# Optimization experiments

Measured on AMD Instinct MI355X. Metric: run time of the kernel, lower is better.

## Reference

```python
import jax, jax.numpy as jnp
import numpy as np

B, LQ, LK = 4, 4096, 4096
D = 1024          # num_heads * key_dim = 16 * 64
Q_DIM = 1024      # query_dim
K_DIM = 1024      # note: linear_k input dim; here inputs carry d_model features
V_DIM = 1024      # value_dim


def setup_inputs() -> dict:
    key = jax.random.key(0)
    ks = jax.random.split(key, 12)
    s_in = 1.0 / np.sqrt(Q_DIM)
    s_d = 1.0 / np.sqrt(D)
    return {
        "q": jax.random.normal(ks[0], (B, LQ, Q_DIM), jnp.float32),
        "k": jax.random.normal(ks[1], (B, LK, K_DIM), jnp.float32),
        "v": jax.random.normal(ks[2], (B, LK, V_DIM), jnp.float32),
        # Linear weights stored [in, out] so projection is x @ W + b
        "Wq": jax.random.normal(ks[3], (Q_DIM, D), jnp.float32) * s_in,
        "bq": jax.random.normal(ks[4], (D,), jnp.float32) * s_in,
        "Wk": jax.random.normal(ks[5], (K_DIM, D), jnp.float32) * s_in,
        "bk": jax.random.normal(ks[6], (D,), jnp.float32) * s_in,
        "Wv": jax.random.normal(ks[7], (V_DIM, D), jnp.float32) * s_in,
        "bv": jax.random.normal(ks[8], (D,), jnp.float32) * s_in,
        "Wo": jax.random.normal(ks[9], (D, V_DIM), jnp.float32) * s_d,
        "bo": jax.random.normal(ks[10], (V_DIM,), jnp.float32) * s_d,
    }


def reference(q, k, v, Wq, bq, Wk, bk, Wv, bv, Wo, bo):
    # Projections: [B, L, D]
    qp = jax.nn.softmax(q @ Wq + bq, axis=-1)   # softmax over feature dim
    kp = jax.nn.softmax(k @ Wk + bk, axis=-2)   # softmax over sequence dim
    vp = jax.nn.softmax(v @ Wv + bv, axis=-2)   # softmax over sequence dim
    # Dropout is identity in eval mode (module uses dropout_p at train only).
    scores = jnp.einsum("bqd,bkd->bqk", qp, kp)  # [B, LQ, LK]
    ctx = jnp.einsum("bqk,bkd->bqd", scores, vp)  # [B, LQ, D]
    return ctx @ Wo + bo                          # [B, LQ, V_DIM]
```

## Files before the change

kernel.cpp:

```cpp
#include <hip/hip_runtime.h>

typedef _Float16 f16x8 __attribute__((ext_vector_type(8)));
typedef float f32x4 __attribute__((ext_vector_type(4)));
typedef long lx2 __attribute__((ext_vector_type(2)));

__device__ __forceinline__ float h2f(unsigned short h) {
  return (float)__builtin_bit_cast(_Float16, h);
}
__device__ __forceinline__ unsigned short f2h(float f) {
  return __builtin_bit_cast(unsigned short, (_Float16)f);
}
__device__ __forceinline__ unsigned char f2e4(float f) {
  unsigned short h = __builtin_bit_cast(unsigned short, (_Float16)f);
  unsigned s = (h >> 8) & 0x80u;
  unsigned ae = h & 0x7FFFu;
  if (ae >= 0x5F00u) return (unsigned char)(s | 0x7Eu);
  if (ae >= 0x2400u) {
    unsigned t = ae - 0x2000u;
    t = (t + 0x3Fu + ((t >> 7) & 1u)) >> 7;
    return (unsigned char)(s | t);
  }
  float v = (float)__builtin_bit_cast(_Float16, (unsigned short)ae) * 512.0f;
  int n = (int)rintf(v);
  return (unsigned char)(s | (unsigned)n);
}
__device__ __forceinline__ unsigned pk4e4(float a, float b, float c, float d) {
  return (unsigned)f2e4(a) | ((unsigned)f2e4(b) << 8) |
         ((unsigned)f2e4(c) << 16) | ((unsigned)f2e4(d) << 24);
}

__device__ __forceinline__ void gload_lds16(const void* g, void* l) {
  __builtin_amdgcn_global_load_lds(
      (const __attribute__((address_space(1))) void*)g,
      (__attribute__((address_space(3))) void*)l, 16, 0, 0);
}

template <int DT, int ASRC, int OUTMODE>
__global__ __launch_bounds__(512, 4) void gemmt(
    const void* __restrict__ Av, const void* __restrict__ Btv,
    void* __restrict__ Cv, const float* __restrict__ bias,
    float* __restrict__ sums,
    int N, int K, int ldk, int gx, int gy, int nsplit,
    long sA, long sB, long sC)
{
  __shared__ alignas(16) unsigned char smem[49152];
  const int tid  = threadIdx.x;
  const int lane = tid & 63;
  const int wave = tid >> 6;
  const int waveM = wave >> 2;
  const int waveN = wave & 3;
  const int EB = (DT == 1) ? 1 : 2;

  const int nwg = (int)gridDim.x;
  const int cpx = nwg >> 3;
  const int wg  = (int)blockIdx.x;
  const int w   = (wg & 7) * cpx + (wg >> 3);
  const int x   = w % gx;
  const int rem = w / gx;
  const int y   = rem % gy;
  const int zt  = rem / gy;
  const int bz  = zt / nsplit;
  const int sp  = zt % nsplit;

  const int m0 = y * 128, n0 = x * 256;
  const size_t ldkB = (size_t)ldk * EB;
  const size_t ldkB64 = ldkB * 64, ldkB128 = ldkB * 128;

  const int srow = tid >> 3;
  const int scol = ((tid * 16) & 127) ^ ((srow & 7) << 4);
  const char* ApR16 = nullptr;
  const char* ApR32 = nullptr;
  const char* BpR;
  {
    const char* Bb = (const char*)Btv + ((long)bz * sB + (long)sp * K) * EB
                     + (size_t)n0 * ldkB;
    BpR = Bb + (size_t)srow * ldkB + scol;
    if (ASRC == 0) {
      const char* Ab = (const char*)Av + ((long)bz * sA + (long)sp * K) * EB
                       + (size_t)m0 * ldkB;
      ApR16 = Ab + (size_t)srow * ldkB + scol;
    } else {
      const char* Ab = (const char*)Av + ((long)bz * sA + (long)sp * K) * 4
                       + (size_t)m0 * (size_t)ldk * 4;
      ApR32 = Ab + (size_t)srow * (size_t)ldk * 4 + (size_t)scol * 2;
    }
  }
  const unsigned oA0 = (unsigned)tid * 16;
  const size_t ldk32_64 = (size_t)ldk * 4 * 64;

  int offA[4], offB[4];
  {
    const int q16 = (lane >> 4) << 4;
#pragma unroll
    for (int mi = 0; mi < 4; ++mi) {
      const int r = waveM * 64 + mi * 16 + (lane & 15);
      offA[mi] = r * 128 + (q16 ^ ((r & 7) << 4));
    }
#pragma unroll
    for (int ni = 0; ni < 4; ++ni) {
      const int r = waveN * 64 + ni * 16 + (lane & 15);
      offB[ni] = 16384 + r * 128 + (q16 ^ ((r & 7) << 4));
    }
  }

  f32x4 acc[4][4] = {};

  float4 pf0, pf1, pf2, pf3;
  if (ASRC == 1) {
    const char* s0 = ApR32;
    const char* s1 = s0 + ldk32_64;
    pf0 = *(const float4*)s0;  pf1 = *(const float4*)(s0 + 16);
    pf2 = *(const float4*)s1;  pf3 = *(const float4*)(s1 + 16);
  }

  const int nk = (DT == 1) ? (K >> 7) : (K >> 6);
  for (int kt = 0; kt < nk; ++kt) {
    const size_t kb = (size_t)kt * 128;
    if (ASRC == 0) {
      gload_lds16(ApR16 + kb,           smem + oA0);
      gload_lds16(ApR16 + ldkB64 + kb,  smem + oA0 + 8192);
    } else {
      unsigned short h0[8], h1[8];
      const float* fa0 = (const float*)&pf0; const float* fa1 = (const float*)&pf1;
      const float* fb0 = (const float*)&pf2; const float* fb1 = (const float*)&pf3;
#pragma unroll
      for (int e = 0; e < 4; ++e) {
        h0[e] = f2h(fa0[e]); h0[4 + e] = f2h(fa1[e]);
        h1[e] = f2h(fb0[e]); h1[4 + e] = f2h(fb1[e]);
      }
      *(uint4*)&smem[oA0]        = *(const uint4*)h0;
      *(uint4*)&smem[oA0 + 8192] = *(const uint4*)h1;
      if (kt + 1 < nk) {
        const char* s0 = ApR32 + (size_t)(kt + 1) * 256;
        const char* s1 = s0 + ldk32_64;
        pf0 = *(const float4*)s0;  pf1 = *(const float4*)(s0 + 16);
        pf2 = *(const float4*)s1;  pf3 = *(const float4*)(s1 + 16);
      }
    }
    gload_lds16(BpR + kb,                     smem + 16384 + oA0);
    gload_lds16(BpR + ldkB64 + kb,            smem + 16384 + oA0 + 8192);
    gload_lds16(BpR + ldkB128 + kb,           smem + 16384 + oA0 + 16384);
    gload_lds16(BpR + ldkB128 + ldkB64 + kb,  smem + 16384 + oA0 + 24576);
    __syncthreads();
#pragma unroll
    for (int kk = 0; kk < 2; ++kk) {
      const int kx = kk << 6;
      if (DT == 0) {
        f16x8 aF[4], bF[4];
#pragma unroll
        for (int mi = 0; mi < 4; ++mi) aF[mi] = *(const f16x8*)&smem[offA[mi] ^ kx];
#pragma unroll
        for (int ni = 0; ni < 4; ++ni) bF[ni] = *(const f16x8*)&smem[offB[ni] ^ kx];
#pragma unroll
        for (int mi = 0; mi < 4; ++mi)
#pragma unroll
          for (int ni = 0; ni < 4; ++ni)
            acc[mi][ni] = __builtin_amdgcn_mfma_f32_16x16x32_f16(aF[mi], bF[ni], acc[mi][ni], 0, 0, 0);
      } else {
        lx2 aF[4], bF[4];
#pragma unroll
        for (int mi = 0; mi < 4; ++mi) aF[mi] = *(const lx2*)&smem[offA[mi] ^ kx];
#pragma unroll
        for (int ni = 0; ni < 4; ++ni) bF[ni] = *(const lx2*)&smem[offB[ni] ^ kx];
#pragma unroll
        for (int h = 0; h < 2; ++h)
#pragma unroll
          for (int mi = 0; mi < 4; ++mi)
#pragma unroll
            for (int ni = 0; ni < 4; ++ni)
              acc[mi][ni] = __builtin_amdgcn_mfma_f32_16x16x32_fp8_fp8(
                  aF[mi][h], bF[ni][h], acc[mi][ni], 0, 0, 0);
      }
    }
    __syncthreads();
  }

  const int rb = (lane >> 4) * 4;
  const int cb_ = lane & 15;
  const long zout = (OUTMODE == 2) ? (long)zt : (long)bz;

  if (OUTMODE == 3) {
#pragma unroll
    for (int m = 0; m < 4; ++m) {
      const int row0 = m0 + waveM * 64 + m * 16 + rb;
      float rs0 = 0, rs1 = 0, rs2 = 0, rs3 = 0;
#pragma unroll
      for (int n = 0; n < 4; ++n) {
        const int col = n0 + waveN * 64 + n * 16 + cb_;
        const float badd = bias[col];
        const float e0 = __expf(acc[m][n][0] + badd);
        const float e1 = __expf(acc[m][n][1] + badd);
        const float e2 = __expf(acc[m][n][2] + badd);
        const float e3 = __expf(acc[m][n][3] + badd);
        unsigned char* C8 = (unsigned char*)Cv + zout * sC;
        C8[(size_t)(row0 + 0) * N + col] = f2e4(e0 * 0.0625f);
        C8[(size_t)(row0 + 1) * N + col] = f2e4(e1 * 0.0625f);
        C8[(size_t)(row0 + 2) * N + col] = f2e4(e2 * 0.0625f);
        C8[(size_t)(row0 + 3) * N + col] = f2e4(e3 * 0.0625f);
        rs0 += e0; rs1 += e1; rs2 += e2; rs3 += e3;
      }
#pragma unroll
      for (int off = 1; off <= 8; off <<= 1) {
        rs0 += __shfl_xor(rs0, off);
        rs1 += __shfl_xor(rs1, off);
        rs2 += __shfl_xor(rs2, off);
        rs3 += __shfl_xor(rs3, off);
      }
      if ((lane & 15) == 0) {
        float* s = sums + (size_t)zout * 4096 + row0;
        atomicAdd(s + 0, rs0);
        atomicAdd(s + 1, rs1);
        atomicAdd(s + 2, rs2);
        atomicAdd(s + 3, rs3);
      }
    }
  } else if (OUTMODE == 4) {
    float cs[4] = {0.f, 0.f, 0.f, 0.f};
#pragma unroll
    for (int m = 0; m < 4; ++m) {
      const int row0 = m0 + waveM * 64 + m * 16 + rb;
#pragma unroll
      for (int n = 0; n < 4; ++n) {
        const int col = n0 + waveN * 64 + n * 16 + cb_;
        const float badd = bias[col];
        float ev[4];
        float ls = 0.f;
#pragma unroll
        for (int r = 0; r < 4; ++r) {
          ev[r] = __expf(acc[m][n][r] + badd);
          ls += ev[r];
        }
        cs[n] += ls;
        *(unsigned*)((unsigned char*)Cv + zout * sC + ((size_t)col << 12) + row0) =
            pk4e4(ev[0] * 0.0625f, ev[1] * 0.0625f, ev[2] * 0.0625f, ev[3] * 0.0625f);
      }
    }
#pragma unroll
    for (int n = 0; n < 4; ++n) {
      cs[n] += __shfl_xor(cs[n], 16);
      cs[n] += __shfl_xor(cs[n], 32);
    }
    if (lane < 16) {
#pragma unroll
      for (int n = 0; n < 4; ++n) {
        const int col = n0 + waveN * 64 + n * 16 + lane;
        atomicAdd(sums + ((size_t)zout << 10) + col, cs[n]);
      }
    }
  } else {
#pragma unroll
    for (int m = 0; m < 4; ++m) {
      const int row0 = m0 + waveM * 64 + m * 16 + rb;
      float i0 = 0, i1 = 0, i2 = 0, i3 = 0;
      if (OUTMODE == 5) {
        const float4 s4 = *(const float4*)&sums[(size_t)zout * 4096 + row0];
        i0 = 1.0f / (256.0f * s4.x); i1 = 1.0f / (256.0f * s4.y);
        i2 = 1.0f / (256.0f * s4.z); i3 = 1.0f / (256.0f * s4.w);
      }
#pragma unroll
      for (int n = 0; n < 4; ++n) {
        const int col = n0 + waveN * 64 + n * 16 + cb_;
        if (OUTMODE == 2) {
#pragma unroll
          for (int r = 0; r < 4; ++r)
            ((unsigned short*)Cv)[zout * sC + (size_t)(row0 + r) * N + col] = f2h(acc[m][n][r]);
        } else if (OUTMODE == 5) {
          const float badd = bias[col];
          float* C32 = (float*)Cv;
          C32[zout * sC + (size_t)(row0 + 0) * N + col] = acc[m][n][0] * i0 + badd;
          C32[zout * sC + (size_t)(row0 + 1) * N + col] = acc[m][n][1] * i1 + badd;
          C32[zout * sC + (size_t)(row0 + 2) * N + col] = acc[m][n][2] * i2 + badd;
          C32[zout * sC + (size_t)(row0 + 3) * N + col] = acc[m][n][3] * i3 + badd;
        } else {
          const float badd = bias[col];
#pragma unroll
          for (int r = 0; r < 4; ++r)
            ((float*)Cv)[zout * sC + (size_t)(row0 + r) * N + col] = acc[m][n][r] + badd;
        }
      }
    }
  }
}

__global__ __launch_bounds__(256) void w_trh4(
    const float* __restrict__ W0, const float* __restrict__ W1,
    const float* __restrict__ W2, const float* __restrict__ W3,
    unsigned short* __restrict__ WTb)
{
  __shared__ unsigned short tile[64][73];
  const int z = blockIdx.z;
  const float* W = (z == 0) ? W0 : (z == 1) ? W1 : (z == 2) ? W2 : W3;
  unsigned short* WT = WTb + (size_t)z * 1024 * 1024;
  const int c0 = blockIdx.x * 64;
  const int r0 = blockIdx.y * 64;
  const int tid = threadIdx.x;
  const int r = tid >> 2;
  const int cq = (tid & 3) * 16;
#pragma unroll
  for (int i = 0; i < 4; ++i) {
    const int c = cq + i * 4;
    const float4 v = *(const float4*)&W[(size_t)(r0 + r) * 1024 + c0 + c];
    tile[r][c + 0] = f2h(v.x);
    tile[r][c + 1] = f2h(v.y);
    tile[r][c + 2] = f2h(v.z);
    tile[r][c + 3] = f2h(v.w);
  }
  __syncthreads();
  const int c = tid >> 2;
  const int rq = (tid & 3) * 16;
  unsigned short outv[16];
#pragma unroll
  for (int j = 0; j < 16; ++j) outv[j] = tile[rq + j][c];
  unsigned short* Tb = WT + (size_t)(c0 + c) * 1024 + r0 + rq;
  ((uint4*)Tb)[0] = ((const uint4*)outv)[0];
  ((uint4*)Tb)[1] = ((const uint4*)outv)[1];
}

__global__ __launch_bounds__(256) void wo8k(
    const unsigned short* __restrict__ WoT, unsigned char* __restrict__ WoT8)
{
  const int i = blockIdx.x * 256 + threadIdx.x;
  const uint2 u = ((const uint2*)WoT)[i];
  ((unsigned*)WoT8)[i] = pk4e4(h2f(u.x & 0xffff) * 8.f, h2f(u.x >> 16) * 8.f,
                               h2f(u.y & 0xffff) * 8.f, h2f(u.y >> 16) * 8.f);
}

__global__ __launch_bounds__(256) void red4m(
    const unsigned short* __restrict__ P, const float* __restrict__ skr,
    const float* __restrict__ svr, unsigned char* __restrict__ O)
{
  const int i = blockIdx.x * 256 + threadIdx.x;
  const int b = i >> 18;
  const int j = i & 262143;
  const int dk = j >> 8;
  const int dv0 = (j & 255) << 2;
  float s0 = 0, s1 = 0, s2 = 0, s3 = 0;
#pragma unroll
  for (int sl = 0; sl < 4; ++sl) {
    const uint2 u = *(const uint2*)(P + (((long)(b * 4 + sl)) << 20) + ((long)j << 2));
    s0 += h2f(u.x & 0xffff); s1 += h2f(u.x >> 16);
    s2 += h2f(u.y & 0xffff); s3 += h2f(u.y >> 16);
  }
  const float fk = 4194304.0f / skr[(b << 10) + dk];
  const float4 fv = *(const float4*)&svr[(b << 10) + dv0];
  ((unsigned*)O)[i] = pk4e4(s0 * fk / fv.x, s1 * fk / fv.y,
                            s2 * fk / fv.z, s3 * fk / fv.w);
}

__global__ __launch_bounds__(256) void red4g(
    const unsigned short* __restrict__ P, unsigned char* __restrict__ O)
{
  const int i = blockIdx.x * 256 + threadIdx.x;
  const int b = i >> 18;
  const int j = i & 262143;
  float s0 = 0, s1 = 0, s2 = 0, s3 = 0;
#pragma unroll
  for (int sl = 0; sl < 4; ++sl) {
    const uint2 u = *(const uint2*)(P + (((long)(b * 4 + sl)) << 20) + ((long)j << 2));
    s0 += h2f(u.x & 0xffff); s1 += h2f(u.x >> 16);
    s2 += h2f(u.y & 0xffff); s3 += h2f(u.y >> 16);
  }
  ((unsigned*)O)[i] = pk4e4(s0 * 0.03125f, s1 * 0.03125f,
                            s2 * 0.03125f, s3 * 0.03125f);
}

extern "C" void kernel_launch(void* const* d_in, const int* in_sizes, int n_in,
                              void* d_out, int out_size, void* d_ws, size_t ws_size,
                              hipStream_t stream) {
  const float* q  = (const float*)d_in[0];
  const float* k  = (const float*)d_in[1];
  const float* v  = (const float*)d_in[2];
  const float* Wq = (const float*)d_in[3];
  const float* bq = (const float*)d_in[4];
  const float* Wk = (const float*)d_in[5];
  const float* bk = (const float*)d_in[6];
  const float* Wv = (const float*)d_in[7];
  const float* bv = (const float*)d_in[8];
  const float* Wo = (const float*)d_in[9];
  const float* bo = (const float*)d_in[10];
  float* out = (float*)d_out;

  char* p = (char*)d_ws;
  unsigned short* Part = (unsigned short*)p; p += 33554432;
  unsigned short* WTb  = (unsigned short*)p; p += 8388608;
  unsigned short* WqT = WTb;
  unsigned short* WkT = WTb + 1L * 1024 * 1024;
  unsigned short* WvT = WTb + 2L * 1024 * 1024;
  unsigned short* WoT = WTb + 3L * 1024 * 1024;
  unsigned char* WoT8 = (unsigned char*)p;   p += 1048576;
  unsigned char* Eq8  = (unsigned char*)p;   p += 16777216;
  unsigned char* ETk8 = (unsigned char*)p;   p += 16777216;
  unsigned char* ETv8 = (unsigned char*)p;   p += 16777216;
  unsigned char* Mh8  = (unsigned char*)p;   p += 4194304;
  unsigned char* GT8  = (unsigned char*)p;   p += 4194304;
  float* sqraw = (float*)p; p += 16384 * 4;
  float* skraw = (float*)p; p += 4096 * 4;
  float* svraw = (float*)p; p += 4096 * 4;

  const dim3 blk(256);
  const dim3 blk512(512);
  const long S22 = 4096L * 1024;
  const long S20 = 1024L * 1024;

  hipMemsetAsync(sqraw, 0, (16384 + 4096 + 4096) * sizeof(float), stream);

  w_trh4<<<dim3(16, 16, 4), blk, 0, stream>>>(Wq, Wk, Wv, Wo, WTb);
  wo8k<<<1024, blk, 0, stream>>>(WoT, WoT8);

  gemmt<0, 1, 3><<<512, blk512, 0, stream>>>(q, WqT, Eq8, bq, sqraw,
      1024, 1024, 1024, 4, 32, 1, S22, 0, S22);

  gemmt<0, 1, 4><<<512, blk512, 0, stream>>>(k, WkT, ETk8, bk, skraw,
      1024, 1024, 1024, 4, 32, 1, S22, 0, S22);

  gemmt<0, 1, 4><<<512, blk512, 0, stream>>>(v, WvT, ETv8, bv, svraw,
      1024, 1024, 1024, 4, 32, 1, S22, 0, S22);

  gemmt<1, 0, 2><<<512, blk512, 0, stream>>>(ETk8, ETv8, Part, nullptr, nullptr,
      1024, 1024, 4096, 4, 8, 4, S22, S22, S20);
  red4m<<<4096, blk, 0, stream>>>(Part, skraw, svraw, Mh8);

  gemmt<1, 0, 2><<<512, blk512, 0, stream>>>(WoT8, Mh8, Part, nullptr, nullptr,
      1024, 256, 1024, 4, 8, 4, 0, S20, S20);
  red4g<<<4096, blk, 0, stream>>>(Part, GT8);

  gemmt<1, 0, 5><<<512, blk512, 0, stream>>>(Eq8, GT8, out, bo, sqraw,
      1024, 1024, 1024, 4, 32, 1, S22, S20, S22);

  (void)in_sizes; (void)n_in; (void)out_size; (void)ws_size;
}
```

Baseline: 280.9 us.

## Merge three projection GEMMs into one launch, use hardware FP8 conversion

Replaces the three separate Q/K/V projection launches with a single proj3 kernel of 1536 workgroups that selects input, weights, bias and epilogue per workgroup. This removes launch gaps and tail effects between the projections. The software float-to-e4m3 conversion is replaced with the cvt_pk_fp8_f32 builtin when the compiler provides it, and the Wo FP8 conversion is folded into the weight transpose kernel, which removes one launch. Risks are small rounding differences from the hardware conversion (saturation and NaN handling) and some divergence from the per-workgroup pointer selection.

Measured after the change: 263.0 us. 1.07x faster.

```diff
diff --git a/kernel.cpp b/kernel.cpp
--- a/kernel.cpp
+++ b/kernel.cpp
@@ -10,7 +10,14 @@
 __device__ __forceinline__ unsigned short f2h(float f) {
   return __builtin_bit_cast(unsigned short, (_Float16)f);
 }
-__device__ __forceinline__ unsigned char f2e4(float f) {
+
+#if __has_builtin(__builtin_amdgcn_cvt_pk_fp8_f32)
+#define HW_FP8 1
+#else
+#define HW_FP8 0
+#endif
+
+__device__ __forceinline__ unsigned char f2e4_sw(float f) {
   unsigned short h = __builtin_bit_cast(unsigned short, (_Float16)f);
   unsigned s = (h >> 8) & 0x80u;
   unsigned ae = h & 0x7FFFu;
@@ -24,9 +31,22 @@
   int n = (int)rintf(v);
   return (unsigned char)(s | (unsigned)n);
 }
+
+__device__ __forceinline__ unsigned pk2e4(float a, float b) {
+#if HW_FP8
+  return (unsigned)__builtin_amdgcn_cvt_pk_fp8_f32(a, b, 0, false) & 0xFFFFu;
+#else
+  return (unsigned)f2e4_sw(a) | ((unsigned)f2e4_sw(b) << 8);
+#endif
+}
 __device__ __forceinline__ unsigned pk4e4(float a, float b, float c, float d) {
-  return (unsigned)f2e4(a) | ((unsigned)f2e4(b) << 8) |
-         ((unsigned)f2e4(c) << 16) | ((unsigned)f2e4(d) << 24);
+#if HW_FP8
+  int lo = __builtin_amdgcn_cvt_pk_fp8_f32(a, b, 0, false);
+  return (unsigned)__builtin_amdgcn_cvt_pk_fp8_f32(c, d, lo, true);
+#else
+  return (unsigned)f2e4_sw(a) | ((unsigned)f2e4_sw(b) << 8) |
+         ((unsigned)f2e4_sw(c) << 16) | ((unsigned)f2e4_sw(d) << 24);
+#endif
 }
 
 __device__ __forceinline__ void gload_lds16(const void* g, void* l) {
@@ -35,11 +55,194 @@
       (__attribute__((address_space(3))) void*)l, 16, 0, 0);
 }
 
-template <int DT, int ASRC, int OUTMODE>
-__global__ __launch_bounds__(512, 4) void gemmt(
-    const void* __restrict__ Av, const void* __restrict__ Btv,
+__global__ __launch_bounds__(512, 4) void proj3(
+    const float* __restrict__ A0, const float* __restrict__ A1,
+    const float* __restrict__ A2, const unsigned short* __restrict__ WTb,
+    const float* __restrict__ b0, const float* __restrict__ b1,
+    const float* __restrict__ b2, unsigned char* __restrict__ C0,
+    unsigned char* __restrict__ C1, unsigned char* __restrict__ C2,
+    float* __restrict__ s0, float* __restrict__ s1, float* __restrict__ s2)
+{
+  __shared__ alignas(16) unsigned char smem[49152];
+  const int tid  = threadIdx.x;
+  const int lane = tid & 63;
+  const int wave = tid >> 6;
+  const int waveM = wave >> 2;
+  const int waveN = wave & 3;
+
+  const int wg = (int)blockIdx.x;
+  const int w  = (wg & 7) * 192 + (wg >> 3);
+  const int z  = w / 512;
+  const int wl = w - z * 512;
+  const int x  = wl & 3;
+  const int rem = wl >> 2;
+  const int y  = rem & 31;
+  const int bz = rem >> 5;
+
+  const float* Af = (z == 0) ? A0 : (z == 1) ? A1 : A2;
+  const float* bi = (z == 0) ? b0 : (z == 1) ? b1 : b2;
+  unsigned char* Cp = (z == 0) ? C0 : (z == 1) ? C1 : C2;
+  float* sums = (z == 0) ? s0 : (z == 1) ? s1 : s2;
+
+  const int m0 = y * 128, n0 = x * 256;
+
+  const int srow = tid >> 3;
+  const int scol = ((tid * 16) & 127) ^ ((srow & 7) << 4);
+  const char* BpR = (const char*)(WTb + (size_t)z * 1048576)
+                    + (size_t)n0 * 2048 + (size_t)srow * 2048 + scol;
+  const char* ApR32 = (const char*)Af + (size_t)bz * (4096L * 1024 * 4)
+                      + (size_t)m0 * 4096 + (size_t)srow * 4096 + (size_t)scol * 2;
+  const unsigned oA0 = (unsigned)tid * 16;
+
+  int offA[4], offB[4];
+  {
+    const int q16 = (lane >> 4) << 4;
+#pragma unroll
+    for (int mi = 0; mi < 4; ++mi) {
+      const int r = waveM * 64 + mi * 16 + (lane & 15);
+      offA[mi] = r * 128 + (q16 ^ ((r & 7) << 4));
+    }
+#pragma unroll
+    for (int ni = 0; ni < 4; ++ni) {
+      const int r = waveN * 64 + ni * 16 + (lane & 15);
+      offB[ni] = 16384 + r * 128 + (q16 ^ ((r & 7) << 4));
+    }
+  }
+
+  f32x4 acc[4][4] = {};
+
+  float4 pf0, pf1, pf2, pf3;
+  {
+    const char* sa = ApR32;
+    const char* sb = sa + 4096 * 64;
+    pf0 = *(const float4*)sa;  pf1 = *(const float4*)(sa + 16);
+    pf2 = *(const float4*)sb;  pf3 = *(const float4*)(sb + 16);
+  }
+
+  for (int kt = 0; kt < 16; ++kt) {
+    const size_t kb = (size_t)kt * 128;
+    {
+      unsigned short h0[8], h1[8];
+      const float* fa0 = (const float*)&pf0; const float* fa1 = (const float*)&pf1;
+      const float* fb0 = (const float*)&pf2; const float* fb1 = (const float*)&pf3;
+#pragma unroll
+      for (int e = 0; e < 4; ++e) {
+        h0[e] = f2h(fa0[e]); h0[4 + e] = f2h(fa1[e]);
+        h1[e] = f2h(fb0[e]); h1[4 + e] = f2h(fb1[e]);
+      }
+      *(uint4*)&smem[oA0]        = *(const uint4*)h0;
+      *(uint4*)&smem[oA0 + 8192] = *(const uint4*)h1;
+      if (kt + 1 < 16) {
+        const char* sa = ApR32 + (size_t)(kt + 1) * 256;
+        const char* sb = sa + 4096 * 64;
+        pf0 = *(const float4*)sa;  pf1 = *(const float4*)(sa + 16);
+        pf2 = *(const float4*)sb;  pf3 = *(const float4*)(sb + 16);
+      }
+    }
+    gload_lds16(BpR + kb,                      smem + 16384 + oA0);
+    gload_lds16(BpR + 2048 * 64 + kb,          smem + 16384 + oA0 + 8192);
+    gload_lds16(BpR + 2048 * 128 + kb,         smem + 16384 + oA0 + 16384);
+    gload_lds16(BpR + 2048 * 192 + kb,         smem + 16384 + oA0 + 24576);
+    __syncthreads();
+#pragma unroll
+    for (int kk = 0; kk < 2; ++kk) {
+      const int kx = kk << 6;
+      f16x8 aF[4], bF[4];
+#pragma unroll
+      for (int mi = 0; mi < 4; ++mi) aF[mi] = *(const f16x8*)&smem[offA[mi] ^ kx];
+#pragma unroll
+      for (int ni = 0; ni < 4; ++ni) bF[ni] = *(const f16x8*)&smem[offB[ni] ^ kx];
+#pragma unroll
+      for (int mi = 0; mi < 4; ++mi)
+#pragma unroll
+        for (int ni = 0; ni < 4; ++ni)
+          acc[mi][ni] = __builtin_amdgcn_mfma_f32_16x16x32_f16(aF[mi], bF[ni], acc[mi][ni], 0, 0, 0);
+    }
+    __syncthreads();
+  }
+
+  const int rb = (lane >> 4) * 4;
+  const int cb_ = lane & 15;
+  const long sC = 4096L * 1024;
+
+  if (z == 0) {
+#pragma unroll
+    for (int m = 0; m < 4; ++m) {
+      const int row0 = m0 + waveM * 64 + m * 16 + rb;
+      float rs0 = 0, rs1 = 0, rs2 = 0, rs3 = 0;
+#pragma unroll
+      for (int n = 0; n < 4; ++n) {
+        const int col = n0 + waveN * 64 + n * 16 + cb_;
+        const float badd = bi[col];
+        const float e0 = __expf(acc[m][n][0] + badd);
+        const float e1 = __expf(acc[m][n][1] + badd);
+        const float e2 = __expf(acc[m][n][2] + badd);
+        const float e3 = __expf(acc[m][n][3] + badd);
+        const unsigned p01 = pk2e4(e0 * 0.0625f, e1 * 0.0625f);
+        const unsigned p23 = pk2e4(e2 * 0.0625f, e3 * 0.0625f);
+        unsigned char* C8 = Cp + (long)bz * sC;
+        C8[(size_t)(row0 + 0) * 1024 + col] = (unsigned char)(p01 & 0xff);
+        C8[(size_t)(row0 + 1) * 1024 + col] = (unsigned char)((p01 >> 8) & 0xff);
+        C8[(size_t)(row0 + 2) * 1024 + col] = (unsigned char)(p23 & 0xff);
+        C8[(size_t)(row0 + 3) * 1024 + col] = (unsigned char)((p23 >> 8) & 0xff);
+        rs0 += e0; rs1 += e1; rs2 += e2; rs3 += e3;
+      }
+#pragma unroll
+      for (int off = 1; off <= 8; off <<= 1) {
+        rs0 += __shfl_xor(rs0, off);
+        rs1 += __shfl_xor(rs1, off);
+        rs2 += __shfl_xor(rs2, off);
+        rs3 += __shfl_xor(rs3, off);
+      }
+      if ((lane & 15) == 0) {
+        float* s = sums + (size_t)bz * 4096 + row0;
+        atomicAdd(s + 0, rs0);
+        atomicAdd(s + 1, rs1);
+        atomicAdd(s + 2, rs2);
+        atomicAdd(s + 3, rs3);
+      }
+    }
+  } else {
+    float cs[4] = {0.f, 0.f, 0.f, 0.f};
+#pragma unroll
+    for (int m = 0; m < 4; ++m) {
+      const int row0 = m0 + waveM * 64 + m * 16 + rb;
+#pragma unroll
+      for (int n = 0; n < 4; ++n) {
+        const int col = n0 + waveN * 64 + n * 16 + cb_;
+        const float badd = bi[col];
+        float ev[4];
+        float ls = 0.f;
+#pragma unroll
+        for (int r = 0; r < 4; ++r) {
+          ev[r] = __expf(acc[m][n][r] + badd);
+          ls += ev[r];
+        }
+        cs[n] += ls;
+        *(unsigned*)(Cp + (long)bz * sC + ((size_t)col << 12) + row0) =
+            pk4e4(ev[0] * 0.0625f, ev[1] * 0.0625f, ev[2] * 0.0625f, ev[3] * 0.0625f);
+      }
+    }
+#pragma unroll
+    for (int n = 0; n < 4; ++n) {
+      cs[n] += __shfl_xor(cs[n], 16);
+      cs[n] += __shfl_xor(cs[n], 32);
+    }
+    if (lane < 16) {
+#pragma unroll
+      for (int n = 0; n < 4; ++n) {
+        const int col = n0 + waveN * 64 + n * 16 + lane;
+        atomicAdd(sums + ((size_t)bz << 10) + col, cs[n]);
+      }
+    }
+  }
+}
+
+template <int OUTMODE>
+__global__ __launch_bounds__(512, 4) void gemm8(
+    const unsigned char* __restrict__ A, const unsigned char* __restrict__ Bt,
     void* __restrict__ Cv, const float* __restrict__ bias,
-    float* __restrict__ sums,
+    const float* __restrict__ sums,
     int N, int K, int ldk, int gx, int gy, int nsplit,
     long sA, long sB, long sC)
 {
@@ -49,7 +252,6 @@
   const int wave = tid >> 6;
   const int waveM = wave >> 2;
   const int waveN = wave & 3;
-  const int EB = (DT == 1) ? 1 : 2;
 
   const int nwg = (int)gridDim.x;
   const int cpx = nwg >> 3;
@@ -63,30 +265,20 @@
   const int sp  = zt % nsplit;
 
   const int m0 = y * 128, n0 = x * 256;
-  const size_t ldkB = (size_t)ldk * EB;
+  const size_t ldkB = (size_t)ldk;
   const size_t ldkB64 = ldkB * 64, ldkB128 = ldkB * 128;
 
   const int srow = tid >> 3;
   const int scol = ((tid * 16) & 127) ^ ((srow & 7) << 4);
-  const char* ApR16 = nullptr;
-  const char* ApR32 = nullptr;
+  const char* ApR;
   const char* BpR;
   {
-    const char* Bb = (const char*)Btv + ((long)bz * sB + (long)sp * K) * EB
-                     + (size_t)n0 * ldkB;
+    const char* Ab = (const char*)A + (long)bz * sA + (long)sp * K + (size_t)m0 * ldkB;
+    const char* Bb = (const char*)Bt + (long)bz * sB + (long)sp * K + (size_t)n0 * ldkB;
+    ApR = Ab + (size_t)srow * ldkB + scol;
     BpR = Bb + (size_t)srow * ldkB + scol;
-    if (ASRC == 0) {
-      const char* Ab = (const char*)Av + ((long)bz * sA + (long)sp * K) * EB
-                       + (size_t)m0 * ldkB;
-      ApR16 = Ab + (size_t)srow * ldkB + scol;
-    } else {
-      const char* Ab = (const char*)Av + ((long)bz * sA + (long)sp * K) * 4
-                       + (size_t)m0 * (size_t)ldk * 4;
-      ApR32 = Ab + (size_t)srow * (size_t)ldk * 4 + (size_t)scol * 2;
-    }
   }
   const unsigned oA0 = (unsigned)tid * 16;
-  const size_t ldk32_64 = (size_t)ldk * 4 * 64;
 
   int offA[4], offB[4];
   {
@@ -105,38 +297,11 @@
 
   f32x4 acc[4][4] = {};
 
-  float4 pf0, pf1, pf2, pf3;
-  if (ASRC == 1) {
-    const char* s0 = ApR32;
-    const char* s1 = s0 + ldk32_64;
-    pf0 = *(const float4*)s0;  pf1 = *(const float4*)(s0 + 16);
-    pf2 = *(const float4*)s1;  pf3 = *(const float4*)(s1 + 16);
-  }
-
-  const int nk = (DT == 1) ? (K >> 7) : (K >> 6);
+  const int nk = K >> 7;
   for (int kt = 0; kt < nk; ++kt) {
     const size_t kb = (size_t)kt * 128;
-    if (ASRC == 0) {
-      gload_lds16(ApR16 + kb,           smem + oA0);
-      gload_lds16(ApR16 + ldkB64 + kb,  smem + oA0 + 8192);
-    } else {
-      unsigned short h0[8], h1[8];
-      const float* fa0 = (const float*)&pf0; const float* fa1 = (const float*)&pf1;
-      const float* fb0 = (const float*)&pf2; const float* fb1 = (const float*)&pf3;
-#pragma unroll
-      for (int e = 0; e < 4; ++e) {
-        h0[e] = f2h(fa0[e]); h0[4 + e] = f2h(fa1[e]);
-        h1[e] = f2h(fb0[e]); h1[4 + e] = f2h(fb1[e]);
-      }
-      *(uint4*)&smem[oA0]        = *(const uint4*)h0;
-      *(uint4*)&smem[oA0 + 8192] = *(const uint4*)h1;
-      if (kt + 1 < nk) {
-        const char* s0 = ApR32 + (size_t)(kt + 1) * 256;
-        const char* s1 = s0 + ldk32_64;
-        pf0 = *(const float4*)s0;  pf1 = *(const float4*)(s0 + 16);
-        pf2 = *(const float4*)s1;  pf3 = *(const float4*)(s1 + 16);
-      }
-    }
+    gload_lds16(ApR + kb,                     smem + oA0);
+    gload_lds16(ApR + ldkB64 + kb,            smem + oA0 + 8192);
     gload_lds16(BpR + kb,                     smem + 16384 + oA0);
     gload_lds16(BpR + ldkB64 + kb,            smem + 16384 + oA0 + 8192);
     gload_lds16(BpR + ldkB128 + kb,           smem + 16384 + oA0 + 16384);
@@ -145,32 +310,19 @@
 #pragma unroll
     for (int kk = 0; kk < 2; ++kk) {
       const int kx = kk << 6;
-      if (DT == 0) {
-        f16x8 aF[4], bF[4];
-#pragma unroll
-        for (int mi = 0; mi < 4; ++mi) aF[mi] = *(const f16x8*)&smem[offA[mi] ^ kx];
-#pragma unroll
-        for (int ni = 0; ni < 4; ++ni) bF[ni] = *(const f16x8*)&smem[offB[ni] ^ kx];
+      lx2 aF[4], bF[4];
+#pragma unroll
+      for (int mi = 0; mi < 4; ++mi) aF[mi] = *(const lx2*)&smem[offA[mi] ^ kx];
+#pragma unroll
+      for (int ni = 0; ni < 4; ++ni) bF[ni] = *(const lx2*)&smem[offB[ni] ^ kx];
+#pragma unroll
+      for (int h = 0; h < 2; ++h)
 #pragma unroll
         for (int mi = 0; mi < 4; ++mi)
 #pragma unroll
           for (int ni = 0; ni < 4; ++ni)
-            acc[mi][ni] = __builtin_amdgcn_mfma_f32_16x16x32_f16(aF[mi], bF[ni], acc[mi][ni], 0, 0, 0);
-      } else {
-        lx2 aF[4], bF[4];
-#pragma unroll
-        for (int mi = 0; mi < 4; ++mi) aF[mi] = *(const lx2*)&smem[offA[mi] ^ kx];
-#pragma unroll
-        for (int ni = 0; ni < 4; ++ni) bF[ni] = *(const lx2*)&smem[offB[ni] ^ kx];
-#pragma unroll
-        for (int h = 0; h < 2; ++h)
-#pragma unroll
-          for (int mi = 0; mi < 4; ++mi)
-#pragma unroll
-            for (int ni = 0; ni < 4; ++ni)
-              acc[mi][ni] = __builtin_amdgcn_mfma_f32_16x16x32_fp8_fp8(
-                  aF[mi][h], bF[ni][h], acc[mi][ni], 0, 0, 0);
-      }
+            acc[mi][ni] = __builtin_amdgcn_mfma_f32_16x16x32_fp8_fp8(
+                aF[mi][h], bF[ni][h], acc[mi][ni], 0, 0, 0);
     }
     __syncthreads();
   }
@@ -178,105 +330,29 @@
   const int rb = (lane >> 4) * 4;
   const int cb_ = lane & 15;
   const long zout = (OUTMODE == 2) ? (long)zt : (long)bz;
-
-  if (OUTMODE == 3) {
-#pragma unroll
-    for (int m = 0; m < 4; ++m) {
-      const int row0 = m0 + waveM * 64 + m * 16 + rb;
-      float rs0 = 0, rs1 = 0, rs2 = 0, rs3 = 0;
-#pragma unroll
-      for (int n = 0; n < 4; ++n) {
-        const int col = n0 + waveN * 64 + n * 16 + cb_;
+#pragma unroll
+  for (int m = 0; m < 4; ++m) {
+    const int row0 = m0 + waveM * 64 + m * 16 + rb;
+    float i0 = 0, i1 = 0, i2 = 0, i3 = 0;
+    if (OUTMODE == 5) {
+      const float4 s4 = *(const float4*)&sums[(size_t)zout * 4096 + row0];
+      i0 = 1.0f / (256.0f * s4.x); i1 = 1.0f / (256.0f * s4.y);
+      i2 = 1.0f / (256.0f * s4.z); i3 = 1.0f / (256.0f * s4.w);
+    }
+#pragma unroll
+    for (int n = 0; n < 4; ++n) {
+      const int col = n0 + waveN * 64 + n * 16 + cb_;
+      if (OUTMODE == 2) {
+#pragma unroll
+        for (int r = 0; r < 4; ++r)
+          ((unsigned short*)Cv)[zout * sC + (size_t)(row0 + r) * N + col] = f2h(acc[m][n][r]);
+      } else {
         const float badd = bias[col];
-        const float e0 = __expf(acc[m][n][0] + badd);
-        const float e1 = __expf(acc[m][n][1] + badd);
-        const float e2 = __expf(acc[m][n][2] + badd);
-        const float e3 = __expf(acc[m][n][3] + badd);
-        unsigned char* C8 = (unsigned char*)Cv + zout * sC;
-        C8[(size_t)(row0 + 0) * N + col] = f2e4(e0 * 0.0625f);
-        C8[(size_t)(row0 + 1) * N + col] = f2e4(e1 * 0.0625f);
-        C8[(size_t)(row0 + 2) * N + col] = f2e4(e2 * 0.0625f);
-        C8[(size_t)(row0 + 3) * N + col] = f2e4(e3 * 0.0625f);
-        rs0 += e0; rs1 += e1; rs2 += e2; rs3 += e3;
-      }
-#pragma unroll
-      for (int off = 1; off <= 8; off <<= 1) {
-        rs0 += __shfl_xor(rs0, off);
-        rs1 += __shfl_xor(rs1, off);
-        rs2 += __shfl_xor(rs2, off);
-        rs3 += __shfl_xor(rs3, off);
-      }
-      if ((lane & 15) == 0) {
-        float* s = sums + (size_t)zout * 4096 + row0;
-        atomicAdd(s + 0, rs0);
-        atomicAdd(s + 1, rs1);
-        atomicAdd(s + 2, rs2);
-        atomicAdd(s + 3, rs3);
-      }
-    }
-  } else if (OUTMODE == 4) {
-    float cs[4] = {0.f, 0.f, 0.f, 0.f};
-#pragma unroll
-    for (int m = 0; m < 4; ++m) {
-      const int row0 = m0 + waveM * 64 + m * 16 + rb;
-#pragma unroll
-      for (int n = 0; n < 4; ++n) {
-        const int col = n0 + waveN * 64 + n * 16 + cb_;
-        const float badd = bias[col];
-        float ev[4];
-        float ls = 0.f;
-#pragma unroll
-        for (int r = 0; r < 4; ++r) {
-          ev[r] = __expf(acc[m][n][r] + badd);
-          ls += ev[r];
-        }
-        cs[n] += ls;
-        *(unsigned*)((unsigned char*)Cv + zout * sC + ((size_t)col << 12) + row0) =
-            pk4e4(ev[0] * 0.0625f, ev[1] * 0.0625f, ev[2] * 0.0625f, ev[3] * 0.0625f);
-      }
-    }
-#pragma unroll
-    for (int n = 0; n < 4; ++n) {
-      cs[n] += __shfl_xor(cs[n], 16);
-      cs[n] += __shfl_xor(cs[n], 32);
-    }
-    if (lane < 16) {
-#pragma unroll
-      for (int n = 0; n < 4; ++n) {
-        const int col = n0 + waveN * 64 + n * 16 + lane;
-        atomicAdd(sums + ((size_t)zout << 10) + col, cs[n]);
-      }
-    }
-  } else {
-#pragma unroll
-    for (int m = 0; m < 4; ++m) {
-      const int row0 = m0 + waveM * 64 + m * 16 + rb;
-      float i0 = 0, i1 = 0, i2 = 0, i3 = 0;
-      if (OUTMODE == 5) {
-        const float4 s4 = *(const float4*)&sums[(size_t)zout * 4096 + row0];
-        i0 = 1.0f / (256.0f * s4.x); i1 = 1.0f / (256.0f * s4.y);
-        i2 = 1.0f / (256.0f * s4.z); i3 = 1.0f / (256.0f * s4.w);
-      }
-#pragma unroll
-      for (int n = 0; n < 4; ++n) {
-        const int col = n0 + waveN * 64 + n * 16 + cb_;
-        if (OUTMODE == 2) {
-#pragma unroll
-          for (int r = 0; r < 4; ++r)
-            ((unsigned short*)Cv)[zout * sC + (size_t)(row0 + r) * N + col] = f2h(acc[m][n][r]);
-        } else if (OUTMODE == 5) {
-          const float badd = bias[col];
-          float* C32 = (float*)Cv;
-          C32[zout * sC + (size_t)(row0 + 0) * N + col] = acc[m][n][0] * i0 + badd;
-          C32[zout * sC + (size_t)(row0 + 1) * N + col] = acc[m][n][1] * i1 + badd;
-          C32[zout * sC + (size_t)(row0 + 2) * N + col] = acc[m][n][2] * i2 + badd;
-          C32[zout * sC + (size_t)(row0 + 3) * N + col] = acc[m][n][3] * i3 + badd;
-        } else {
-          const float badd = bias[col];
-#pragma unroll
-          for (int r = 0; r < 4; ++r)
-            ((float*)Cv)[zout * sC + (size_t)(row0 + r) * N + col] = acc[m][n][r] + badd;
-        }
+        float* C32 = (float*)Cv;
+        C32[zout * sC + (size_t)(row0 + 0) * N + col] = acc[m][n][0] * i0 + badd;
+        C32[zout * sC + (size_t)(row0 + 1) * N + col] = acc[m][n][1] * i1 + badd;
+        C32[zout * sC + (size_t)(row0 + 2) * N + col] = acc[m][n][2] * i2 + badd;
+        C32[zout * sC + (size_t)(row0 + 3) * N + col] = acc[m][n][3] * i3 + badd;
       }
     }
   }
@@ -285,7 +361,7 @@
 __global__ __launch_bounds__(256) void w_trh4(
     const float* __restrict__ W0, const float* __restrict__ W1,
     const float* __restrict__ W2, const float* __restrict__ W3,
-    unsigned short* __restrict__ WTb)
+    unsigned short* __restrict__ WTb, unsigned char* __restrict__ WoT8)
 {
   __shared__ unsigned short tile[64][73];
   const int z = blockIdx.z;
@@ -314,15 +390,14 @@
   unsigned short* Tb = WT + (size_t)(c0 + c) * 1024 + r0 + rq;
   ((uint4*)Tb)[0] = ((const uint4*)outv)[0];
   ((uint4*)Tb)[1] = ((const uint4*)outv)[1];
-}
-
-__global__ __launch_bounds__(256) void wo8k(
-    const unsigned short* __restrict__ WoT, unsigned char* __restrict__ WoT8)
-{
-  const int i = blockIdx.x * 256 + threadIdx.x;
-  const uint2 u = ((const uint2*)WoT)[i];
-  ((unsigned*)WoT8)[i] = pk4e4(h2f(u.x & 0xffff) * 8.f, h2f(u.x >> 16) * 8.f,
-                               h2f(u.y & 0xffff) * 8.f, h2f(u.y >> 16) * 8.f);
+  if (z == 3) {
+    unsigned u4[4];
+#pragma unroll
+    for (int j = 0; j < 4; ++j)
+      u4[j] = pk4e4(h2f(outv[4 * j + 0]) * 8.f, h2f(outv[4 * j + 1]) * 8.f,
+                    h2f(outv[4 * j + 2]) * 8.f, h2f(outv[4 * j + 3]) * 8.f);
+    *(uint4*)(WoT8 + (size_t)(c0 + c) * 1024 + r0 + rq) = *(const uint4*)u4;
+  }
 }
 
 __global__ __launch_bounds__(256) void red4m(
@@ -383,10 +458,6 @@
   char* p = (char*)d_ws;
   unsigned short* Part = (unsigned short*)p; p += 33554432;
   unsigned short* WTb  = (unsigned short*)p; p += 8388608;
-  unsigned short* WqT = WTb;
-  unsigned short* WkT = WTb + 1L * 1024 * 1024;
-  unsigned short* WvT = WTb + 2L * 1024 * 1024;
-  unsigned short* WoT = WTb + 3L * 1024 * 1024;
   unsigned char* WoT8 = (unsigned char*)p;   p += 1048576;
   unsigned char* Eq8  = (unsigned char*)p;   p += 16777216;
   unsigned char* ETk8 = (unsigned char*)p;   p += 16777216;
@@ -404,27 +475,20 @@
 
   hipMemsetAsync(sqraw, 0, (16384 + 4096 + 4096) * sizeof(float), stream);
 
-  w_trh4<<<dim3(16, 16, 4), blk, 0, stream>>>(Wq, Wk, Wv, Wo, WTb);
-  wo8k<<<1024, blk, 0, stream>>>(WoT, WoT8);
-
-  gemmt<0, 1, 3><<<512, blk512, 0, stream>>>(q, WqT, Eq8, bq, sqraw,
-      1024, 1024, 1024, 4, 32, 1, S22, 0, S22);
-
-  gemmt<0, 1, 4><<<512, blk512, 0, stream>>>(k, WkT, ETk8, bk, skraw,
-      1024, 1024, 1024, 4, 32, 1, S22, 0, S22);
-
-  gemmt<0, 1, 4><<<512, blk512, 0, stream>>>(v, WvT, ETv8, bv, svraw,
-      1024, 1024, 1024, 4, 32, 1, S22, 0, S22);
-
-  gemmt<1, 0, 2><<<512, blk512, 0, stream>>>(ETk8, ETv8, Part, nullptr, nullptr,
+  w_trh4<<<dim3(16, 16, 4), blk, 0, stream>>>(Wq, Wk, Wv, Wo, WTb, WoT8);
+
+  proj3<<<1536, blk512, 0, stream>>>(q, k, v, WTb, bq, bk, bv,
+                                     Eq8, ETk8, ETv8, sqraw, skraw, svraw);
+
+  gemm8<2><<<512, blk512, 0, stream>>>(ETk8, ETv8, Part, nullptr, nullptr,
       1024, 1024, 4096, 4, 8, 4, S22, S22, S20);
   red4m<<<4096, blk, 0, stream>>>(Part, skraw, svraw, Mh8);
 
-  gemmt<1, 0, 2><<<512, blk512, 0, stream>>>(WoT8, Mh8, Part, nullptr, nullptr,
+  gemm8<2><<<512, blk512, 0, stream>>>(WoT8, Mh8, Part, nullptr, nullptr,
       1024, 256, 1024, 4, 8, 4, 0, S20, S20);
   red4g<<<4096, blk, 0, stream>>>(Part, GT8);
 
-  gemmt<1, 0, 5><<<512, blk512, 0, stream>>>(Eq8, GT8, out, bo, sqraw,
+  gemm8<5><<<512, blk512, 0, stream>>>(Eq8, GT8, out, bo, sqraw,
       1024, 1024, 1024, 4, 32, 1, S22, S20, S22);
 
   (void)in_sizes; (void)n_in; (void)out_size; (void)ws_size;
```
